# Kernel optimization log

Hardware: AMD Instinct MI355X
Metric: run time of the kernel (lower is better)

Reference implementation:

```python
import jax, jax.numpy as jnp
import numpy as np

EPS = 1e-8


def _pairwise_cosine(x, y):
    # F.cosine_similarity clamps each norm to eps before dividing.
    xn = x / jnp.maximum(jnp.linalg.norm(x, axis=-1, keepdims=True), EPS)
    yn = y / jnp.maximum(jnp.linalg.norm(y, axis=-1, keepdims=True), EPS)
    # torch layout: sim[i, j] = cos(y[i], x[j]) -> [N, N]
    return jnp.einsum('id,jd->ij', yn, xn)


def _kl_loss(target_logits, predicted_logits):
    t = jax.nn.softmax(target_logits, axis=-1)
    log_t = jax.nn.log_softmax(target_logits, axis=-1)
    log_p = jax.nn.log_softmax(predicted_logits, axis=-1)
    kl = jnp.sum(t * (log_t - log_p), axis=-1)
    return jnp.mean(kl)


def setup_inputs() -> dict:
    key = jax.random.key(0)
    k1, k2 = jax.random.split(key)
    N, D = 4096, 1024
    target = jax.random.normal(k1, (N, D), dtype=jnp.float32)
    predicted = jax.random.normal(k2, (N, D), dtype=jnp.float32)
    return {"target": target, "predicted": predicted}


def reference(target, predicted):
    x1 = _pairwise_cosine(target, target)      # [N, N]
    x2 = _pairwise_cosine(predicted, predicted)
    return _kl_loss(x1, x2) + _kl_loss(target, predicted)
```

## Files before the change

kernel.cpp:

```cpp
#include <hip/hip_runtime.h>
#include <hip/hip_bf16.h>
#include <math.h>

#define N 4096
#define D 1024
#define PANEL 128
#define NPANEL 32
#define NTRI (NPANEL * (NPANEL + 1) / 2)
#define BK 32
#define NITER (D / BK)
#define PANBYTES 131072

typedef float f32x4 __attribute__((ext_vector_type(4)));


__global__ void zero_kernel(float* p) {
  int i = blockIdx.x * 256 + threadIdx.x;
  if (i < N * 3) p[i] = 0.0f;
}

__global__ __launch_bounds__(256) void prep_kernel(const float* __restrict__ tgt,
                                                   const float* __restrict__ prd,
                                                   uint8_t* __restrict__ tn,
                                                   uint8_t* __restrict__ pn,
                                                   float* __restrict__ rowkl) {
  const int wid = threadIdx.x >> 6, lane = threadIdx.x & 63;
  const int row = blockIdx.x * 4 + wid;
  const float* tr = tgt + (size_t)row * D;
  const float* pr = prd + (size_t)row * D;
  float4 tv[4], pv[4];
  #pragma unroll
  for (int j = 0; j < 4; j++) {
    tv[j] = ((const float4*)tr)[j * 64 + lane];
    pv[j] = ((const float4*)pr)[j * 64 + lane];
  }
  float ss_t = 0.f, ss_p = 0.f, mx_t = -1e30f, mx_p = -1e30f;
  #pragma unroll
  for (int j = 0; j < 4; j++) {
    float t_[4] = {tv[j].x, tv[j].y, tv[j].z, tv[j].w};
    float p_[4] = {pv[j].x, pv[j].y, pv[j].z, pv[j].w};
    #pragma unroll
    for (int k = 0; k < 4; k++) {
      ss_t += t_[k] * t_[k]; ss_p += p_[k] * p_[k];
      mx_t = fmaxf(mx_t, t_[k]); mx_p = fmaxf(mx_p, p_[k]);
    }
  }
  #pragma unroll
  for (int o = 32; o > 0; o >>= 1) {
    ss_t += __shfl_xor(ss_t, o);
    ss_p += __shfl_xor(ss_p, o);
    mx_t = fmaxf(mx_t, __shfl_xor(mx_t, o));
    mx_p = fmaxf(mx_p, __shfl_xor(mx_p, o));
  }
  float rnt = 1.0f / fmaxf(sqrtf(ss_t), 1e-8f);
  float rnp = 1.0f / fmaxf(sqrtf(ss_p), 1e-8f);

  const int P = row >> 7, r = row & 127;
  const int kcsub = lane >> 3;
  const int G = (lane & 7) >> 1;
  const int Gs = G ^ ((r >> 2) & 3);
  const int bphys = (Gs << 3) | ((lane & 1) * 4);

  float et = 0.f, ep = 0.f, sv = 0.f;
  #pragma unroll
  for (int j = 0; j < 4; j++) {
    float t_[4] = {tv[j].x, tv[j].y, tv[j].z, tv[j].w};
    float p_[4] = {pv[j].x, pv[j].y, pv[j].z, pv[j].w};
    uint32_t tpack = 0, ppack = 0;
    tpack = __builtin_amdgcn_cvt_pk_fp8_f32(t_[0] * rnt, t_[1] * rnt, tpack, false);
    tpack = __builtin_amdgcn_cvt_pk_fp8_f32(t_[2] * rnt, t_[3] * rnt, tpack, true);
    ppack = __builtin_amdgcn_cvt_pk_fp8_f32(p_[0] * rnp, p_[1] * rnp, ppack, false);
    ppack = __builtin_amdgcn_cvt_pk_fp8_f32(p_[2] * rnp, p_[3] * rnp, ppack, true);
    size_t off = ((size_t)(P * 32 + j * 8 + kcsub)) * 4096 + r * 32 + bphys;
    *(uint32_t*)(tn + off) = tpack;
    *(uint32_t*)(pn + off) = ppack;
    #pragma unroll
    for (int k = 0; k < 4; k++) {
      float e = __expf(t_[k] - mx_t);
      et += e; sv += e * (t_[k] - p_[k]);
      ep += __expf(p_[k] - mx_p);
    }
  }
  #pragma unroll
  for (int o = 32; o > 0; o >>= 1) {
    et += __shfl_xor(et, o);
    ep += __shfl_xor(ep, o);
    sv += __shfl_xor(sv, o);
  }
  if (lane == 0)
    rowkl[row] = sv / et - (mx_t - mx_p + __logf(et) - __logf(ep));
}

__global__ __launch_bounds__(256, 2) void gram_kernel(const uint8_t* __restrict__ tn,
                                                      const uint8_t* __restrict__ pn,
                                                      float* __restrict__ rowstats) {
  const int tid = threadIdx.x;
  const int wid = tid >> 6, lane = tid & 63;
  const int g = lane >> 4, lr = lane & 15;
  const int wr = wid >> 1, wc = wid & 1;

  int p = (blockIdx.x & 7) * (NTRI / 8) + (blockIdx.x >> 3);
  int rem = p, R = 0, C = 0;
  bool found = false;
  for (R = 0; R < 4 && !found; R++) {
    for (C = R; C < 4; C++) {
      int sz = (R == C) ? 36 : 64;
      if (rem < sz) { found = true; break; }
      rem -= sz;
    }
  }
  R--;
  int pr, pc;
  if (R == C) {
    pr = 0;
    while (rem >= 8 - pr) { rem -= 8 - pr; pr++; }
    pc = pr + rem;
  } else {
    pr = rem >> 3; pc = rem & 7;
  }
  const int rb = R * 8 + pr, cc = C * 8 + pc;
  const int rowbase = rb * PANEL, colbase = cc * PANEL;

  const uint32_t sw = (lr >> 2) & 3;
  const uint32_t fo = (uint32_t)lr * 32 + ((g ^ sw) << 3);
  const uint32_t offA = (uint32_t)wr * 2048 + fo;
  const uint32_t offB = (uint32_t)wc * 2048 + fo;
  const uint8_t* baseA0 = tn + (size_t)rb * PANBYTES + offA;
  const uint8_t* baseA1 = pn + (size_t)rb * PANBYTES + offA;
  const uint8_t* baseB0 = tn + (size_t)cc * PANBYTES + offB;
  const uint8_t* baseB1 = pn + (size_t)cc * PANBYTES + offB;

  f32x4 acc[4][4][2];
  #pragma unroll
  for (int rt = 0; rt < 4; rt++)
    #pragma unroll
    for (int ct = 0; ct < 4; ct++)
      #pragma unroll
      for (int m = 0; m < 2; m++)
        acc[rt][ct][m] = (f32x4){0.f, 0.f, 0.f, 0.f};

  long a0[4][2], b0[4][2], a1[4][2], b1[4][2];

#define LOADSET(aS, bS, kc)                                                \
  {                                                                        \
    const uint32_t ko = (uint32_t)(kc) * 4096;                             \
    _Pragma("unroll")                                                      \
    for (int rt = 0; rt < 4; rt++) {                                       \
      aS[rt][0] = *(const long*)(baseA0 + ko + rt * 512);                  \
      aS[rt][1] = *(const long*)(baseA1 + ko + rt * 512);                  \
    }                                                                      \
    _Pragma("unroll")                                                      \
    for (int ct = 0; ct < 4; ct++) {                                       \
      bS[ct][0] = *(const long*)(baseB0 + ko + ct * 512);                  \
      bS[ct][1] = *(const long*)(baseB1 + ko + ct * 512);                  \
    }                                                                      \
  }

#define BODYSET(aS, bS)                                                    \
  _Pragma("unroll")                                                        \
  for (int ct = 0; ct < 4; ct++)                                           \
    _Pragma("unroll")                                                      \
    for (int m = 0; m < 2; m++)                                            \
      _Pragma("unroll")                                                    \
      for (int rt = 0; rt < 4; rt++)                                       \
        acc[rt][ct][m] = __builtin_amdgcn_mfma_f32_16x16x32_fp8_fp8(       \
            aS[rt][m], bS[ct][m], acc[rt][ct][m], 0, 0, 0);

  LOADSET(a0, b0, 0);
  for (int k = 0; k < NITER; k += 2) {
    LOADSET(a1, b1, k + 1);
    BODYSET(a0, b0);
    if (k + 2 < NITER) LOADSET(a0, b0, k + 2);
    BODYSET(a1, b1);
  }
#undef LOADSET
#undef BODYSET

  #pragma unroll
  for (int rt = 0; rt < 4; rt++) {
    #pragma unroll
    for (int r = 0; r < 4; r++) {
      float e1 = 0.f, e2 = 0.f, sl = 0.f;
      #pragma unroll
      for (int ct = 0; ct < 4; ct++) {
        float s1 = acc[rt][ct][0][r], s2 = acc[rt][ct][1][r];
        float pw = __expf(s1 - 1.0f);
        e1 += pw; sl += pw * (s1 - s2);
        e2 += __expf(s2 - 1.0f);
      }
      #pragma unroll
      for (int mk = 1; mk < 16; mk <<= 1) {
        e1 += __shfl_xor(e1, mk);
        e2 += __shfl_xor(e2, mk);
        sl += __shfl_xor(sl, mk);
      }
      if (lr == 0) {
        int row = rowbase + wr * 64 + rt * 16 + g * 4 + r;
        atomicAdd(&rowstats[row * 3 + 0], e1);
        atomicAdd(&rowstats[row * 3 + 1], e2);
        atomicAdd(&rowstats[row * 3 + 2], sl);
      }
    }
  }
  if (rb != cc) {
    #pragma unroll
    for (int ct = 0; ct < 4; ct++) {
      float e1 = 0.f, e2 = 0.f, sl = 0.f;
      #pragma unroll
      for (int rt = 0; rt < 4; rt++)
        #pragma unroll
        for (int r = 0; r < 4; r++) {
          float s1 = acc[rt][ct][0][r], s2 = acc[rt][ct][1][r];
          float pw = __expf(s1 - 1.0f);
          e1 += pw; sl += pw * (s1 - s2);
          e2 += __expf(s2 - 1.0f);
        }
      e1 += __shfl_xor(e1, 16); e2 += __shfl_xor(e2, 16); sl += __shfl_xor(sl, 16);
      e1 += __shfl_xor(e1, 32); e2 += __shfl_xor(e2, 32); sl += __shfl_xor(sl, 32);
      if (g == 0) {
        int col = colbase + wc * 64 + ct * 16 + lr;
        atomicAdd(&rowstats[col * 3 + 0], e1);
        atomicAdd(&rowstats[col * 3 + 1], e2);
        atomicAdd(&rowstats[col * 3 + 2], sl);
      }
    }
  }
}

__global__ __launch_bounds__(1024) void finalize_kernel(const float* __restrict__ rowstats,
                                                        const float* __restrict__ rowkl,
                                                        float* __restrict__ out) {
  __shared__ float buf[16];
  float s = 0.f;
  for (int r = threadIdx.x; r < N; r += 1024) {
    float e1 = rowstats[r * 3 + 0];
    float e2 = rowstats[r * 3 + 1];
    float sl = rowstats[r * 3 + 2];
    s += sl / e1 - (__logf(e1) - __logf(e2)) + rowkl[r];
  }
  #pragma unroll
  for (int o = 32; o > 0; o >>= 1) s += __shfl_xor(s, o);
  if ((threadIdx.x & 63) == 0) buf[threadIdx.x >> 6] = s;
  __syncthreads();
  if (threadIdx.x == 0) {
    float t = 0.f;
    #pragma unroll
    for (int i = 0; i < 16; i++) t += buf[i];
    out[0] = t * (1.0f / (float)N);
  }
}

extern "C" void kernel_launch(void* const* d_in, const int* in_sizes, int n_in,
                              void* d_out, int out_size, void* d_ws, size_t ws_size,
                              hipStream_t stream) {
  const float* tgt = (const float*)d_in[0];
  const float* prd = (const float*)d_in[1];
  float* out = (float*)d_out;
  char* ws = (char*)d_ws;
  uint8_t* tn = (uint8_t*)ws;
  uint8_t* pn = (uint8_t*)(ws + 4194304);
  float* rowstats = (float*)(ws + 8388608);
  float* rowkl = rowstats + N * 3;

  zero_kernel<<<(N * 3 + 255) / 256, 256, 0, stream>>>(rowstats);
  prep_kernel<<<N / 4, 256, 0, stream>>>(tgt, prd, tn, pn, rowkl);
  gram_kernel<<<NTRI, 256, 0, stream>>>(tn, pn, rowstats);
  finalize_kernel<<<1, 1024, 0, stream>>>(rowstats, rowkl, out);
}
```

Before: 105.9 us.

## Split target and predicted Gram products across separate waves per block

The gram kernel now launches 512 threads per block. Waves 0-3 compute the target-panel product and waves 4-7 compute the predicted-panel product, each holding half the accumulators. Target results are staged through 64KB of shared memory so the predicted waves can run the fused softmax/KL epilogue. This cuts per-thread register pressure to raise occupancy and memory-latency hiding, at the cost of a block-wide barrier, shared-memory traffic and half the waves sitting idle during the epilogue.

```diff
diff --git a/kernel.cpp b/kernel.cpp
--- a/kernel.cpp
+++ b/kernel.cpp
@@ -7,8 +7,7 @@
 #define PANEL 128
 #define NPANEL 32
 #define NTRI (NPANEL * (NPANEL + 1) / 2)
-#define BK 32
-#define NITER (D / BK)
+#define NITER 32
 #define PANBYTES 131072
 
 typedef float f32x4 __attribute__((ext_vector_type(4)));
@@ -91,13 +90,15 @@
     rowkl[row] = sv / et - (mx_t - mx_p + __logf(et) - __logf(ep));
 }
 
-__global__ __launch_bounds__(256, 2) void gram_kernel(const uint8_t* __restrict__ tn,
+__global__ __launch_bounds__(512, 4) void gram_kernel(const uint8_t* __restrict__ tn,
                                                       const uint8_t* __restrict__ pn,
                                                       float* __restrict__ rowstats) {
+  __shared__ float s1buf[4][64][64];
   const int tid = threadIdx.x;
   const int wid = tid >> 6, lane = tid & 63;
   const int g = lane >> 4, lr = lane & 15;
-  const int wr = wid >> 1, wc = wid & 1;
+  const int mat = wid >> 2;
+  const int wr = (wid >> 1) & 1, wc = wid & 1;
 
   int p = (blockIdx.x & 7) * (NTRI / 8) + (blockIdx.x >> 3);
   int rem = p, R = 0, C = 0;
@@ -123,48 +124,37 @@
 
   const uint32_t sw = (lr >> 2) & 3;
   const uint32_t fo = (uint32_t)lr * 32 + ((g ^ sw) << 3);
-  const uint32_t offA = (uint32_t)wr * 2048 + fo;
-  const uint32_t offB = (uint32_t)wc * 2048 + fo;
-  const uint8_t* baseA0 = tn + (size_t)rb * PANBYTES + offA;
-  const uint8_t* baseA1 = pn + (size_t)rb * PANBYTES + offA;
-  const uint8_t* baseB0 = tn + (size_t)cc * PANBYTES + offB;
-  const uint8_t* baseB1 = pn + (size_t)cc * PANBYTES + offB;
-
-  f32x4 acc[4][4][2];
+  const uint8_t* base = mat ? pn : tn;
+  const uint8_t* baseA = base + (size_t)rb * PANBYTES + (uint32_t)wr * 2048 + fo;
+  const uint8_t* baseB = base + (size_t)cc * PANBYTES + (uint32_t)wc * 2048 + fo;
+
+  f32x4 acc[4][4];
   #pragma unroll
   for (int rt = 0; rt < 4; rt++)
     #pragma unroll
     for (int ct = 0; ct < 4; ct++)
-      #pragma unroll
-      for (int m = 0; m < 2; m++)
-        acc[rt][ct][m] = (f32x4){0.f, 0.f, 0.f, 0.f};
-
-  long a0[4][2], b0[4][2], a1[4][2], b1[4][2];
-
-#define LOADSET(aS, bS, kc)                                                \
-  {                                                                        \
-    const uint32_t ko = (uint32_t)(kc) * 4096;                             \
-    _Pragma("unroll")                                                      \
-    for (int rt = 0; rt < 4; rt++) {                                       \
-      aS[rt][0] = *(const long*)(baseA0 + ko + rt * 512);                  \
-      aS[rt][1] = *(const long*)(baseA1 + ko + rt * 512);                  \
-    }                                                                      \
-    _Pragma("unroll")                                                      \
-    for (int ct = 0; ct < 4; ct++) {                                       \
-      bS[ct][0] = *(const long*)(baseB0 + ko + ct * 512);                  \
-      bS[ct][1] = *(const long*)(baseB1 + ko + ct * 512);                  \
-    }                                                                      \
-  }
-
-#define BODYSET(aS, bS)                                                    \
-  _Pragma("unroll")                                                        \
-  for (int ct = 0; ct < 4; ct++)                                           \
-    _Pragma("unroll")                                                      \
-    for (int m = 0; m < 2; m++)                                            \
-      _Pragma("unroll")                                                    \
-      for (int rt = 0; rt < 4; rt++)                                       \
-        acc[rt][ct][m] = __builtin_amdgcn_mfma_f32_16x16x32_fp8_fp8(       \
-            aS[rt][m], bS[ct][m], acc[rt][ct][m], 0, 0, 0);
+      acc[rt][ct] = (f32x4){0.f, 0.f, 0.f, 0.f};
+
+  long a0[4], b0[4], a1[4], b1[4];
+
+#define LOADSET(aS, bS, kc)                                  \
+  {                                                          \
+    const uint32_t ko = (uint32_t)(kc) * 4096;               \
+    _Pragma("unroll")                                        \
+    for (int rt = 0; rt < 4; rt++)                           \
+      aS[rt] = *(const long*)(baseA + ko + rt * 512);        \
+    _Pragma("unroll")                                        \
+    for (int ct = 0; ct < 4; ct++)                           \
+      bS[ct] = *(const long*)(baseB + ko + ct * 512);        \
+  }
+
+#define BODYSET(aS, bS)                                      \
+  _Pragma("unroll")                                          \
+  for (int ct = 0; ct < 4; ct++)                             \
+    _Pragma("unroll")                                        \
+    for (int rt = 0; rt < 4; rt++)                           \
+      acc[rt][ct] = __builtin_amdgcn_mfma_f32_16x16x32_fp8_fp8( \
+          aS[rt], bS[ct], acc[rt][ct], 0, 0, 0);
 
   LOADSET(a0, b0, 0);
   for (int k = 0; k < NITER; k += 2) {
@@ -176,52 +166,67 @@
 #undef LOADSET
 #undef BODYSET
 
-  #pragma unroll
-  for (int rt = 0; rt < 4; rt++) {
-    #pragma unroll
-    for (int r = 0; r < 4; r++) {
-      float e1 = 0.f, e2 = 0.f, sl = 0.f;
+  float (*q)[64] = s1buf[wr * 2 + wc];
+  if (mat == 0) {
+    #pragma unroll
+    for (int rt = 0; rt < 4; rt++)
       #pragma unroll
-      for (int ct = 0; ct < 4; ct++) {
-        float s1 = acc[rt][ct][0][r], s2 = acc[rt][ct][1][r];
-        float pw = __expf(s1 - 1.0f);
-        e1 += pw; sl += pw * (s1 - s2);
-        e2 += __expf(s2 - 1.0f);
-      }
+      for (int ct = 0; ct < 4; ct++)
+        #pragma unroll
+        for (int r = 0; r < 4; r++)
+          q[rt * 16 + g * 4 + r][ct * 16 + lr] = acc[rt][ct][r];
+  }
+  __syncthreads();
+  if (mat == 1) {
+    #pragma unroll
+    for (int rt = 0; rt < 4; rt++) {
       #pragma unroll
-      for (int mk = 1; mk < 16; mk <<= 1) {
-        e1 += __shfl_xor(e1, mk);
-        e2 += __shfl_xor(e2, mk);
-        sl += __shfl_xor(sl, mk);
-      }
-      if (lr == 0) {
-        int row = rowbase + wr * 64 + rt * 16 + g * 4 + r;
-        atomicAdd(&rowstats[row * 3 + 0], e1);
-        atomicAdd(&rowstats[row * 3 + 1], e2);
-        atomicAdd(&rowstats[row * 3 + 2], sl);
-      }
-    }
-  }
-  if (rb != cc) {
-    #pragma unroll
-    for (int ct = 0; ct < 4; ct++) {
-      float e1 = 0.f, e2 = 0.f, sl = 0.f;
-      #pragma unroll
-      for (int rt = 0; rt < 4; rt++)
-        #pragma unroll
-        for (int r = 0; r < 4; r++) {
-          float s1 = acc[rt][ct][0][r], s2 = acc[rt][ct][1][r];
+      for (int r = 0; r < 4; r++) {
+        float e1 = 0.f, e2 = 0.f, sl = 0.f;
+        #pragma unroll
+        for (int ct = 0; ct < 4; ct++) {
+          float s1 = q[rt * 16 + g * 4 + r][ct * 16 + lr];
+          float s2 = acc[rt][ct][r];
           float pw = __expf(s1 - 1.0f);
           e1 += pw; sl += pw * (s1 - s2);
           e2 += __expf(s2 - 1.0f);
         }
-      e1 += __shfl_xor(e1, 16); e2 += __shfl_xor(e2, 16); sl += __shfl_xor(sl, 16);
-      e1 += __shfl_xor(e1, 32); e2 += __shfl_xor(e2, 32); sl += __shfl_xor(sl, 32);
-      if (g == 0) {
-        int col = colbase + wc * 64 + ct * 16 + lr;
-        atomicAdd(&rowstats[col * 3 + 0], e1);
-        atomicAdd(&rowstats[col * 3 + 1], e2);
-        atomicAdd(&rowstats[col * 3 + 2], sl);
+        #pragma unroll
+        for (int mk = 1; mk < 16; mk <<= 1) {
+          e1 += __shfl_xor(e1, mk);
+          e2 += __shfl_xor(e2, mk);
+          sl += __shfl_xor(sl, mk);
+        }
+        if (lr == 0) {
+          int row = rowbase + wr * 64 + rt * 16 + g * 4 + r;
+          atomicAdd(&rowstats[row * 3 + 0], e1);
+          atomicAdd(&rowstats[row * 3 + 1], e2);
+          atomicAdd(&rowstats[row * 3 + 2], sl);
+        }
+      }
+    }
+    if (rb != cc) {
+      #pragma unroll
+      for (int ct = 0; ct < 4; ct++) {
+        float e1 = 0.f, e2 = 0.f, sl = 0.f;
+        #pragma unroll
+        for (int rt = 0; rt < 4; rt++)
+          #pragma unroll
+          for (int r = 0; r < 4; r++) {
+            float s1 = q[rt * 16 + g * 4 + r][ct * 16 + lr];
+            float s2 = acc[rt][ct][r];
+            float pw = __expf(s1 - 1.0f);
+            e1 += pw; sl += pw * (s1 - s2);
+            e2 += __expf(s2 - 1.0f);
+          }
+        e1 += __shfl_xor(e1, 16); e2 += __shfl_xor(e2, 16); sl += __shfl_xor(sl, 16);
+        e1 += __shfl_xor(e1, 32); e2 += __shfl_xor(e2, 32); sl += __shfl_xor(sl, 32);
+        if (g == 0) {
+          int col = colbase + wc * 64 + ct * 16 + lr;
+          atomicAdd(&rowstats[col * 3 + 0], e1);
+          atomicAdd(&rowstats[col * 3 + 1], e2);
+          atomicAdd(&rowstats[col * 3 + 2], sl);
+        }
       }
     }
   }
@@ -264,6 +269,6 @@
 
   zero_kernel<<<(N * 3 + 255) / 256, 256, 0, stream>>>(rowstats);
   prep_kernel<<<N / 4, 256, 0, stream>>>(tgt, prd, tn, pn, rowkl);
-  gram_kernel<<<NTRI, 256, 0, stream>>>(tn, pn, rowstats);
+  gram_kernel<<<NTRI, 512, 0, stream>>>(tn, pn, rowstats);
   finalize_kernel<<<1, 1024, 0, stream>>>(rowstats, rowkl, out);
 }
```

Result: slower. 141.2 us (+33.4%).
